# Optimization experiments

Measured on AMD Instinct MI355X. Metric: run time of the kernel, lower is better.

The kernel has to match this reference:

```python
import jax, jax.numpy as jnp
import numpy as np

EMBEDDING_DIM = 256
CODEBOOK_SIZE = 1024
COMMITMENT_COST = 0.25


def setup_inputs() -> dict:
    key = jax.random.key(0)
    k1, k2 = jax.random.split(key)
    inputs = jax.random.normal(k1, (16, 4096, EMBEDDING_DIM), dtype=jnp.float32)
    embeddings = jax.random.normal(k2, (EMBEDDING_DIM, CODEBOOK_SIZE), dtype=jnp.float32)
    return {"inputs": inputs, "embeddings": embeddings}


def reference(inputs, embeddings):
    # inputs: [B, T, D]; embeddings: [D, K]
    D = embeddings.shape[0]
    K = embeddings.shape[1]
    flat = inputs.reshape(-1, D)  # [N, D]

    sim = flat @ embeddings
    dists = (jnp.sum(flat * flat, axis=1, keepdims=True)
             + jnp.sum(embeddings * embeddings, axis=0)
             - 2.0 * sim)
    flat_idx = jnp.argmin(dists, axis=1)  # [N]

    encodings = jax.nn.one_hot(flat_idx, K, dtype=jnp.float32)  # [N, K]
    encoding_indices = flat_idx.reshape(inputs.shape[:-1])  # [B, T]

    # embedding lookup: gather rows of embeddings^T -> [B, T, D]
    quantized = jnp.take(embeddings.T, encoding_indices, axis=0)

    e_latent_loss = jnp.mean(jnp.square(jax.lax.stop_gradient(quantized) - inputs))
    q_latent_loss = jnp.mean(jnp.square(quantized - jax.lax.stop_gradient(inputs)))
    loss = q_latent_loss + COMMITMENT_COST * e_latent_loss

    # straight-through estimator
    quantized_st = inputs + jax.lax.stop_gradient(quantized - inputs)

    return quantized_st, encodings, encoding_indices, loss
```

## Files before the change

kernel.cpp:

```cpp
#include <hip/hip_runtime.h>

#define N_ROWS 65536
#define DIM    256
#define KCB    1024

#define Q_OFF    0
#define ENC_OFF  (N_ROWS * DIM)
#define IDX_OFF  (ENC_OFF + N_ROWS * KCB)
#define LOSS_OFF (IDX_OFF + N_ROWS)

#define ET_OFF   (ENC_OFF + 0)
#define NRM_OFF  (ENC_OFF + 262144)
#define IDXI_OFF (ENC_OFF + 263168)
#define PART_OFF (ENC_OFF + 328704)
#define AMB_OFF  (ENC_OFF + 345088)
#define PMIN_OFF (ENC_OFF + 524288)
#define A2_OFF   (ENC_OFF + 4718592)
#define BST_OFF  (ENC_OFF + 21495808)

#define TAU 0.05f
#define MAXCAND 20000
#define MAXFB   16000

typedef short  bf16x8 __attribute__((ext_vector_type(8)));
typedef float  f32x4  __attribute__((ext_vector_type(4)));
typedef unsigned short u16x8 __attribute__((ext_vector_type(8)));
#define AS1 __attribute__((address_space(1)))
#define AS3 __attribute__((address_space(3)))

__device__ inline unsigned short f2bf(float x) {
    unsigned u = __float_as_uint(x);
    return (unsigned short)((u + 0x7FFFu + ((u >> 16) & 1u)) >> 16);
}
__device__ inline float bf2f(unsigned short b) {
    return __uint_as_float(((unsigned)b) << 16);
}

__global__ __launch_bounds__(256)
void vq_prep_a(const float* __restrict__ X, float* __restrict__ out) {
    unsigned short* A2 = (unsigned short*)(out + A2_OFF);
    int gid = blockIdx.x * 256 + threadIdx.x;
    int row = gid >> 5;
    int d0  = (gid & 31) * 8;
    const float* xp = X + (size_t)row * DIM + d0;
    float4 v0 = *(const float4*)xp;
    float4 v1 = *(const float4*)(xp + 4);
    float xv[8] = {v0.x, v0.y, v0.z, v0.w, v1.x, v1.y, v1.z, v1.w};
    u16x8 h, l;
#pragma unroll
    for (int i = 0; i < 8; ++i) {
        unsigned short hb = f2bf(xv[i]);
        h[i] = hb;
        l[i] = f2bf(xv[i] - bf2f(hb));
    }
    *(u16x8*)(A2 + (size_t)row * 512 + d0) = h;
    *(u16x8*)(A2 + (size_t)row * 512 + 256 + d0) = l;
}

__global__ __launch_bounds__(64)
void vq_prep_b(const float* __restrict__ E, float* __restrict__ out) {
    float* ET  = out + ET_OFF;
    float* nrm = out + NRM_OFF;
    unsigned short* B2 = (unsigned short*)(out + BST_OFF);
    const int k = blockIdx.x, t = threadIdx.x;
    float v[4]; float s = 0.f;
    ushort4 hb, lb;
#pragma unroll
    for (int i = 0; i < 4; ++i) {
        float e = E[(size_t)(t * 4 + i) * KCB + k];
        v[i] = e; s += e * e;
        unsigned short h = f2bf(e);
        ((unsigned short*)&hb)[i] = h;
        ((unsigned short*)&lb)[i] = f2bf(e - bf2f(h));
    }
    *(float4*)(ET + (size_t)k * DIM + t * 4) = *(float4*)v;
    *(ushort4*)(B2 + (size_t)k * 512 + t * 4) = hb;
    *(ushort4*)(B2 + (size_t)k * 512 + 256 + t * 4) = lb;
#pragma unroll
    for (int off = 32; off >= 1; off >>= 1) s += __shfl_xor(s, off);
    if (t == 0) nrm[k] = s;
    if (k == 0 && t == 0) { int* a = (int*)(out + AMB_OFF); a[0] = 0; a[1] = 0; }
}

__global__ __launch_bounds__(256, 3)
void vq_gemm(float* __restrict__ out) {
    __shared__ short lds[24576];
    const unsigned short* A2 = (const unsigned short*)(out + A2_OFF);
    const unsigned short* B2 = (const unsigned short*)(out + BST_OFF);
    const float* nrm = out + NRM_OFF;
    float4* pmin = (float4*)(out + PMIN_OFF);

    const int orig = blockIdx.x;
    const int mapped = (orig & 7) * 512 + (orig >> 3);
    const int rb = mapped >> 3, cb = mapped & 7;
    const int row0 = rb * 128, col0 = cb * 128;

    const int tid = threadIdx.x;
    const int lane = tid & 63, l15 = lane & 15, lhi = lane >> 4;
    const int w = tid >> 6, wr = w >> 1, wc = w & 1;
    const int swz = (l15 & 7) * 8;

    f32x4 acc[4][4];
#pragma unroll
    for (int i = 0; i < 4; ++i)
#pragma unroll
        for (int j = 0; j < 4; ++j) acc[i][j] = (f32x4){0.f, 0.f, 0.f, 0.f};

    const int sr   = tid >> 3;
    const int sksw = ((tid & 7) ^ ((tid >> 3) & 7)) * 8;
    const int wofs = (tid & 192) * 16;

#define STAGE4(SRC, R0, KOFF, LDSB)                                           \
    _Pragma("unroll")                                                         \
    for (int i = 0; i < 4; ++i) {                                             \
        __builtin_amdgcn_global_load_lds(                                     \
            (const AS1 unsigned*)((SRC) + (size_t)((R0) + i * 32 + sr) * 512  \
                                  + (KOFF) + sksw),                           \
            (AS3 unsigned*)((char*)lds + (LDSB) + i * 4096 + wofs), 16, 0, 0);\
    }

    for (int kr = 0; kr < 4; ++kr) {
        __syncthreads();
        STAGE4(A2, row0, kr * 64, 0);
        STAGE4(B2, col0, kr * 64, 16384);
        STAGE4(B2, col0, 256 + kr * 64, 32768);
        asm volatile("s_waitcnt vmcnt(0)" ::: "memory");
        __syncthreads();
#pragma unroll
        for (int kk = 0; kk < 2; ++kk) {
            const int cofs = (kk * 32 + lhi * 8) ^ swz;
            bf16x8 af[4], bf[4];
#pragma unroll
            for (int mi = 0; mi < 4; ++mi)
                af[mi] = *(const bf16x8*)&lds[(wr * 64 + mi * 16 + l15) * 64 + cofs];
#pragma unroll
            for (int ni = 0; ni < 4; ++ni)
                bf[ni] = *(const bf16x8*)&lds[8192 + (wc * 64 + ni * 16 + l15) * 64 + cofs];
#pragma unroll
            for (int mi = 0; mi < 4; ++mi)
#pragma unroll
                for (int ni = 0; ni < 4; ++ni)
                    acc[mi][ni] = __builtin_amdgcn_mfma_f32_16x16x32_bf16(
                        af[mi], bf[ni], acc[mi][ni], 0, 0, 0);
#pragma unroll
            for (int ni = 0; ni < 4; ++ni)
                bf[ni] = *(const bf16x8*)&lds[16384 + (wc * 64 + ni * 16 + l15) * 64 + cofs];
#pragma unroll
            for (int mi = 0; mi < 4; ++mi)
#pragma unroll
                for (int ni = 0; ni < 4; ++ni)
                    acc[mi][ni] = __builtin_amdgcn_mfma_f32_16x16x32_bf16(
                        af[mi], bf[ni], acc[mi][ni], 0, 0, 0);
        }
    }
    for (int kr = 0; kr < 4; ++kr) {
        __syncthreads();
        STAGE4(A2, row0, 256 + kr * 64, 0);
        STAGE4(B2, col0, kr * 64, 16384);
        asm volatile("s_waitcnt vmcnt(0)" ::: "memory");
        __syncthreads();
#pragma unroll
        for (int kk = 0; kk < 2; ++kk) {
            const int cofs = (kk * 32 + lhi * 8) ^ swz;
            bf16x8 af[4], bf[4];
#pragma unroll
            for (int mi = 0; mi < 4; ++mi)
                af[mi] = *(const bf16x8*)&lds[(wr * 64 + mi * 16 + l15) * 64 + cofs];
#pragma unroll
            for (int ni = 0; ni < 4; ++ni)
                bf[ni] = *(const bf16x8*)&lds[8192 + (wc * 64 + ni * 16 + l15) * 64 + cofs];
#pragma unroll
            for (int mi = 0; mi < 4; ++mi)
#pragma unroll
                for (int ni = 0; ni < 4; ++ni)
                    acc[mi][ni] = __builtin_amdgcn_mfma_f32_16x16x32_bf16(
                        af[mi], bf[ni], acc[mi][ni], 0, 0, 0);
        }
    }
#undef STAGE4

    float nv[4];
#pragma unroll
    for (int ni = 0; ni < 4; ++ni) nv[ni] = nrm[col0 + wc * 64 + ni * 16 + l15];
#pragma unroll
    for (int mi = 0; mi < 4; ++mi)
#pragma unroll
        for (int j = 0; j < 4; ++j) {
            float a = 3.4e38f, b = 3.4e38f; int ia = 0, ib = 0;
#pragma unroll
            for (int ni = 0; ni < 4; ++ni) {
                float dist = fmaf(-2.f, acc[mi][ni][j], nv[ni]);
                int col = col0 + wc * 64 + ni * 16 + l15;
                if (dist < a) { b = a; ib = ia; a = dist; ia = col; }
                else if (dist < b) { b = dist; ib = col; }
            }
#pragma unroll
            for (int off = 1; off < 16; off <<= 1) {
                float oa = __shfl_xor(a, off), ob = __shfl_xor(b, off);
                int   oi = __shfl_xor(ia, off), oj = __shfl_xor(ib, off);
                if (oa < a || (oa == a && oi < ia)) {
                    if (a < ob || (a == ob && ia < oj)) { b = a; ib = ia; }
                    else { b = ob; ib = oj; }
                    a = oa; ia = oi;
                } else {
                    if (oa < b || (oa == b && oi < ib)) { b = oa; ib = oi; }
                }
            }
            if (l15 == 0) {
                int grow = row0 + wr * 64 + mi * 16 + lhi * 4 + j;
                float4 pv;
                pv.x = a; pv.y = __int_as_float(ia);
                pv.z = b; pv.w = __int_as_float(ib);
                pmin[(size_t)grow * 16 + cb * 2 + wc] = pv;
            }
        }
}

__global__ __launch_bounds__(256)
void vq_combine(float* __restrict__ out) {
    const float4* pmin = (const float4*)(out + PMIN_OFF);
    int* idxi = (int*)(out + IDXI_OFF);
    int* amb  = (int*)(out + AMB_OFF);
    int* fb   = (int*)(out + PART_OFF);
    const int row = blockIdx.x * 256 + threadIdx.x;
    float v1[16], v2[16]; int i1[16], i2[16];
    float a = 3.4e38f, b = 3.4e38f; int ia = 0;
#pragma unroll
    for (int s = 0; s < 16; ++s) {
        float4 p = pmin[(size_t)row * 16 + s];
        v1[s] = p.x; i1[s] = __float_as_int(p.y);
        v2[s] = p.z; i2[s] = __float_as_int(p.w);
        if (v1[s] < a || (v1[s] == a && i1[s] < ia)) { b = fminf(a, v2[s]); a = v1[s]; ia = i1[s]; }
        else b = fminf(b, v1[s]);
    }
    idxi[row] = ia;
    if (b - a < TAU) {
        const float lim = a + TAU;
        int cands[6]; int nc = 0; bool ok = true;
#pragma unroll
        for (int s = 0; s < 16; ++s) {
            if (v1[s] < lim) { if (nc < 6) cands[nc] = i1[s]; ++nc; }
            if (v2[s] < lim) { if (nc < 6) cands[nc] = i2[s]; ++nc; ok = false; }
        }
        if (ok && nc <= 6) {
            int pos = atomicAdd(&amb[0], 1);
            if (pos < MAXCAND) {
                int* e = amb + 16 + pos * 8;
                e[0] = row; e[1] = nc;
#pragma unroll
                for (int c = 0; c < 6; ++c) e[2 + c] = (c < nc) ? cands[c] : 0;
            } else ok = false;
        } else ok = false;
        if (!ok) {
            int pos = atomicAdd(&amb[1], 1);
            if (pos < MAXFB) fb[pos] = row;
        }
    }
}

__global__ __launch_bounds__(256)
void vq_rescore_cand(const float* __restrict__ X, float* __restrict__ out) {
    const float* ET  = out + ET_OFF;
    const float* nrm = out + NRM_OFF;
    const int* amb = (const int*)(out + AMB_OFF);
    int* idxi = (int*)(out + IDXI_OFF);
    int count = amb[0]; if (count > MAXCAND) count = MAXCAND;
    for (int it = blockIdx.x * 256 + threadIdx.x; it < count; it += gridDim.x * 256) {
        const int* e = amb + 16 + it * 8;
        const int row = e[0], nc = e[1];
        const float* xp = X + (size_t)row * DIM;
        float best = 3.4e38f; int bi = 0x7fffffff;
        for (int c = 0; c < nc; ++c) {
            const int code = e[2 + c];
            const float* ep = ET + (size_t)code * DIM;
            float acc = 0.f;
#pragma unroll 8
            for (int d = 0; d < 256; ++d)
                acc = fmaf(xp[d], ep[d], acc);
            float dist = fmaf(-2.f, acc, nrm[code]);
            if (dist < best || (dist == best && code < bi)) { best = dist; bi = code; }
        }
        idxi[row] = bi;
    }
}

__global__ __launch_bounds__(256)
void vq_rescore_fb(const float* __restrict__ X, float* __restrict__ out) {
    __shared__ float xs[4][256];
    const float* ET  = out + ET_OFF;
    const float* nrm = out + NRM_OFF;
    const int* amb = (const int*)(out + AMB_OFF);
    const int* fb  = (const int*)(out + PART_OFF);
    int* idxi = (int*)(out + IDXI_OFF);
    const int wid = threadIdx.x >> 6, lane = threadIdx.x & 63;
    int count = amb[1]; if (count > MAXFB) count = MAXFB;
    for (int it = blockIdx.x * 4 + wid; it < count; it += gridDim.x * 4) {
        const int row = fb[it];
        *(float4*)&xs[wid][lane * 4] = *(const float4*)(X + (size_t)row * DIM + lane * 4);
        float best = 3.4e38f; int bi = 0;
        for (int cc = 0; cc < 16; ++cc) {
            const int code = cc * 64 + lane;
            const float* ep = ET + (size_t)code * DIM;
            float acc = 0.f;
#pragma unroll
            for (int d = 0; d < 256; d += 4) {
                float4 ev = *(const float4*)(ep + d);
                acc = fmaf(xs[wid][d],     ev.x, acc);
                acc = fmaf(xs[wid][d + 1], ev.y, acc);
                acc = fmaf(xs[wid][d + 2], ev.z, acc);
                acc = fmaf(xs[wid][d + 3], ev.w, acc);
            }
            float dist = fmaf(-2.f, acc, nrm[code]);
            if (dist < best) { best = dist; bi = code; }
        }
#pragma unroll
        for (int off = 1; off < 64; off <<= 1) {
            float ov = __shfl_xor(best, off);
            int   oi = __shfl_xor(bi, off);
            if (ov < best || (ov == best && oi < bi)) { best = ov; bi = oi; }
        }
        if (lane == 0) idxi[row] = bi;
    }
}

__global__ __launch_bounds__(256)
void vq_outputs(const float* __restrict__ X, float* __restrict__ out) {
    const float* ET  = out + ET_OFF;
    const int*   idx = (const int*)(out + IDXI_OFF);
    float*       part = out + PART_OFF;
    __shared__ float red[4];
    const int row  = blockIdx.x * 4 + (threadIdx.x >> 6);
    const int lane = threadIdx.x & 63;
    const int id   = idx[row];
    float4 e = *(const float4*)(ET + (size_t)id * DIM + lane * 4);
    float4 x = *(const float4*)(X + (size_t)row * DIM + lane * 4);
    float dx = e.x - x.x, dy = e.y - x.y, dz = e.z - x.z, dw = e.w - x.w;
    float4 q;
    q.x = x.x + dx; q.y = x.y + dy; q.z = x.z + dz; q.w = x.w + dw;
    *(float4*)(out + Q_OFF + (size_t)row * DIM + lane * 4) = q;
    float s = dx * dx + dy * dy + dz * dz + dw * dw;
#pragma unroll
    for (int off = 32; off >= 1; off >>= 1) s += __shfl_xor(s, off);
    if (lane == 0) {
        red[threadIdx.x >> 6] = s;
        out[IDX_OFF + row] = (float)id;
    }
    __syncthreads();
    if (threadIdx.x == 0) part[blockIdx.x] = red[0] + red[1] + red[2] + red[3];
}

__global__ __launch_bounds__(256)
void vq_loss(float* __restrict__ out) {
    const float* part = out + PART_OFF;
    __shared__ double red[256];
    const int tid = threadIdx.x;
    double s = 0.0;
    for (int i = tid; i < 16384; i += 256) s += (double)part[i];
    red[tid] = s;
    __syncthreads();
    for (int off = 128; off > 0; off >>= 1) {
        if (tid < off) red[tid] += red[tid + off];
        __syncthreads();
    }
    if (tid == 0)
        out[LOSS_OFF] = (float)(1.25 * red[0] / (double)((size_t)N_ROWS * DIM));
}

__global__ __launch_bounds__(256)
void vq_encodings(float* __restrict__ out) {
    const float* idxf = out + IDX_OFF;
    float4* enc4 = (float4*)(out + ENC_OFF);
    const size_t total4 = (size_t)N_ROWS * KCB / 4;
    const size_t stride = (size_t)gridDim.x * blockDim.x;
    for (size_t g = (size_t)blockIdx.x * blockDim.x + threadIdx.x; g < total4; g += stride) {
        int n  = (int)(g >> 8);
        int c0 = ((int)g & 255) * 4;
        int r  = (int)idxf[n] - c0;
        float4 v;
        v.x = (r == 0) ? 1.f : 0.f;
        v.y = (r == 1) ? 1.f : 0.f;
        v.z = (r == 2) ? 1.f : 0.f;
        v.w = (r == 3) ? 1.f : 0.f;
        enc4[g] = v;
    }
}

extern "C" void kernel_launch(void* const* d_in, const int* in_sizes, int n_in,
                              void* d_out, int out_size, void* d_ws, size_t ws_size,
                              hipStream_t stream) {
    const float* X = (const float*)d_in[0];
    const float* E = (const float*)d_in[1];
    float* out = (float*)d_out;

    vq_prep_a      <<<8192, 256, 0, stream>>>(X, out);
    vq_prep_b      <<<1024,  64, 0, stream>>>(E, out);
    vq_gemm        <<<4096, 256, 0, stream>>>(out);
    vq_combine     <<<256,  256, 0, stream>>>(out);
    vq_rescore_cand<<<64,   256, 0, stream>>>(X, out);
    vq_rescore_fb  <<<128,  256, 0, stream>>>(X, out);
    vq_outputs     <<<16384, 256, 0, stream>>>(X, out);
    vq_loss        <<<1,    256, 0, stream>>>(out);
    vq_encodings   <<<2048, 256, 0, stream>>>(out);
}
```

Before: 755.7 us.

## Drop second-best index tracking and load hi/lo codebook fragments together in GEMM

The GEMM inner loop now loads the hi and lo bf16 codebook fragments up front instead of reloading one register set between MFMA batches. The epilogue reduction stops tracking the second-best index and carries only the second-best value, which cuts shuffles and branches. The combine kernel no longer keeps 16-entry register arrays and rereads the partial minima from memory when a row is ambiguous. The candidate rescore launch is widened from 64 to 256 blocks. Together these aim to lower register pressure and epilogue cost, at the price of more live fragment registers in the main loop and a second read of the partial minima.

Result: faster. 733.6 us (-2.9%).

```diff
diff --git a/kernel.cpp b/kernel.cpp
--- a/kernel.cpp
+++ b/kernel.cpp
@@ -129,28 +129,27 @@
 #pragma unroll
         for (int kk = 0; kk < 2; ++kk) {
             const int cofs = (kk * 32 + lhi * 8) ^ swz;
-            bf16x8 af[4], bf[4];
+            bf16x8 af[4], bh[4], bl[4];
 #pragma unroll
             for (int mi = 0; mi < 4; ++mi)
                 af[mi] = *(const bf16x8*)&lds[(wr * 64 + mi * 16 + l15) * 64 + cofs];
 #pragma unroll
-            for (int ni = 0; ni < 4; ++ni)
-                bf[ni] = *(const bf16x8*)&lds[8192 + (wc * 64 + ni * 16 + l15) * 64 + cofs];
+            for (int ni = 0; ni < 4; ++ni) {
+                bh[ni] = *(const bf16x8*)&lds[8192 + (wc * 64 + ni * 16 + l15) * 64 + cofs];
+                bl[ni] = *(const bf16x8*)&lds[16384 + (wc * 64 + ni * 16 + l15) * 64 + cofs];
+            }
 #pragma unroll
             for (int mi = 0; mi < 4; ++mi)
 #pragma unroll
                 for (int ni = 0; ni < 4; ++ni)
                     acc[mi][ni] = __builtin_amdgcn_mfma_f32_16x16x32_bf16(
-                        af[mi], bf[ni], acc[mi][ni], 0, 0, 0);
-#pragma unroll
-            for (int ni = 0; ni < 4; ++ni)
-                bf[ni] = *(const bf16x8*)&lds[16384 + (wc * 64 + ni * 16 + l15) * 64 + cofs];
+                        af[mi], bh[ni], acc[mi][ni], 0, 0, 0);
 #pragma unroll
             for (int mi = 0; mi < 4; ++mi)
 #pragma unroll
                 for (int ni = 0; ni < 4; ++ni)
                     acc[mi][ni] = __builtin_amdgcn_mfma_f32_16x16x32_bf16(
-                        af[mi], bf[ni], acc[mi][ni], 0, 0, 0);
+                        af[mi], bl[ni], acc[mi][ni], 0, 0, 0);
         }
     }
     for (int kr = 0; kr < 4; ++kr) {
@@ -162,19 +161,19 @@
 #pragma unroll
         for (int kk = 0; kk < 2; ++kk) {
             const int cofs = (kk * 32 + lhi * 8) ^ swz;
-            bf16x8 af[4], bf[4];
+            bf16x8 af[4], bh[4];
 #pragma unroll
             for (int mi = 0; mi < 4; ++mi)
                 af[mi] = *(const bf16x8*)&lds[(wr * 64 + mi * 16 + l15) * 64 + cofs];
 #pragma unroll
             for (int ni = 0; ni < 4; ++ni)
-                bf[ni] = *(const bf16x8*)&lds[8192 + (wc * 64 + ni * 16 + l15) * 64 + cofs];
+                bh[ni] = *(const bf16x8*)&lds[8192 + (wc * 64 + ni * 16 + l15) * 64 + cofs];
 #pragma unroll
             for (int mi = 0; mi < 4; ++mi)
 #pragma unroll
                 for (int ni = 0; ni < 4; ++ni)
                     acc[mi][ni] = __builtin_amdgcn_mfma_f32_16x16x32_bf16(
-                        af[mi], bf[ni], acc[mi][ni], 0, 0, 0);
+                        af[mi], bh[ni], acc[mi][ni], 0, 0, 0);
         }
     }
 #undef STAGE4
@@ -186,31 +185,26 @@
     for (int mi = 0; mi < 4; ++mi)
 #pragma unroll
         for (int j = 0; j < 4; ++j) {
-            float a = 3.4e38f, b = 3.4e38f; int ia = 0, ib = 0;
+            float a = 3.4e38f, b = 3.4e38f; int ia = 0;
 #pragma unroll
             for (int ni = 0; ni < 4; ++ni) {
                 float dist = fmaf(-2.f, acc[mi][ni][j], nv[ni]);
                 int col = col0 + wc * 64 + ni * 16 + l15;
-                if (dist < a) { b = a; ib = ia; a = dist; ia = col; }
-                else if (dist < b) { b = dist; ib = col; }
+                if (dist < a) { b = a; a = dist; ia = col; }
+                else if (dist < b) b = dist;
             }
 #pragma unroll
             for (int off = 1; off < 16; off <<= 1) {
-                float oa = __shfl_xor(a, off), ob = __shfl_xor(b, off);
-                int   oi = __shfl_xor(ia, off), oj = __shfl_xor(ib, off);
-                if (oa < a || (oa == a && oi < ia)) {
-                    if (a < ob || (a == ob && ia < oj)) { b = a; ib = ia; }
-                    else { b = ob; ib = oj; }
-                    a = oa; ia = oi;
-                } else {
-                    if (oa < b || (oa == b && oi < ib)) { b = oa; ib = oi; }
-                }
+                float oa = __shfl_xor(a, off);
+                float ob = __shfl_xor(b, off);
+                int   oi = __shfl_xor(ia, off);
+                if (oa < a || (oa == a && oi < ia)) { b = fminf(a, ob); a = oa; ia = oi; }
+                else b = fminf(b, oa);
             }
             if (l15 == 0) {
                 int grow = row0 + wr * 64 + mi * 16 + lhi * 4 + j;
                 float4 pv;
-                pv.x = a; pv.y = __int_as_float(ia);
-                pv.z = b; pv.w = __int_as_float(ib);
+                pv.x = a; pv.y = __int_as_float(ia); pv.z = b; pv.w = 0.f;
                 pmin[(size_t)grow * 16 + cb * 2 + wc] = pv;
             }
         }
@@ -223,15 +217,13 @@
     int* amb  = (int*)(out + AMB_OFF);
     int* fb   = (int*)(out + PART_OFF);
     const int row = blockIdx.x * 256 + threadIdx.x;
-    float v1[16], v2[16]; int i1[16], i2[16];
     float a = 3.4e38f, b = 3.4e38f; int ia = 0;
 #pragma unroll
     for (int s = 0; s < 16; ++s) {
         float4 p = pmin[(size_t)row * 16 + s];
-        v1[s] = p.x; i1[s] = __float_as_int(p.y);
-        v2[s] = p.z; i2[s] = __float_as_int(p.w);
-        if (v1[s] < a || (v1[s] == a && i1[s] < ia)) { b = fminf(a, v2[s]); a = v1[s]; ia = i1[s]; }
-        else b = fminf(b, v1[s]);
+        float v1 = p.x; int i1 = __float_as_int(p.y);
+        if (v1 < a || (v1 == a && i1 < ia)) { b = fminf(a, p.z); a = v1; ia = i1; }
+        else b = fminf(b, v1);
     }
     idxi[row] = ia;
     if (b - a < TAU) {
@@ -239,8 +231,9 @@
         int cands[6]; int nc = 0; bool ok = true;
 #pragma unroll
         for (int s = 0; s < 16; ++s) {
-            if (v1[s] < lim) { if (nc < 6) cands[nc] = i1[s]; ++nc; }
-            if (v2[s] < lim) { if (nc < 6) cands[nc] = i2[s]; ++nc; ok = false; }
+            float4 p = pmin[(size_t)row * 16 + s];
+            if (p.z < lim) ok = false;
+            if (p.x < lim) { if (nc < 6) cands[nc] = __float_as_int(p.y); ++nc; }
         }
         if (ok && nc <= 6) {
             int pos = atomicAdd(&amb[0], 1);
@@ -396,7 +389,7 @@
     vq_prep_b      <<<1024,  64, 0, stream>>>(E, out);
     vq_gemm        <<<4096, 256, 0, stream>>>(out);
     vq_combine     <<<256,  256, 0, stream>>>(out);
-    vq_rescore_cand<<<64,   256, 0, stream>>>(X, out);
+    vq_rescore_cand<<<256,  256, 0, stream>>>(X, out);
     vq_rescore_fb  <<<128,  256, 0, stream>>>(X, out);
     vq_outputs     <<<16384, 256, 0, stream>>>(X, out);
     vq_loss        <<<1,    256, 0, stream>>>(out);
```
